# Optimization experiments

Measured on AMD Instinct MI355X. Metric: run time of the kernel, lower is better.

## Reference

```python
import jax, jax.numpy as jnp
from jax import lax
import numpy as np

B, C, H, W = 8, 32, 512, 256
HEAD = 64
NUM_PEAKS, RADIUS, THRESH = 18, 5, 0.1
BN_EPS = 1e-5


def setup_inputs() -> dict:
    key = jax.random.key(0)
    ks = jax.random.split(key, 8)
    f32 = jnp.float32
    return {
        "x": jax.random.normal(ks[0], (B, C, H, W), f32),
        # fc_hm head params
        "w1_hm": jax.random.normal(ks[1], (HEAD, C, 3, 3), f32) * 0.05,
        "b1_hm": jnp.zeros((HEAD,), f32),
        "g_hm": jnp.ones((HEAD,), f32),
        "be_hm": jnp.zeros((HEAD,), f32),
        "m_hm": jnp.zeros((HEAD,), f32),
        "v_hm": jnp.ones((HEAD,), f32),
        "w2_hm": jax.random.normal(ks[2], (2, HEAD, 1, 1), f32) * 0.05,
        "b2_hm": jnp.zeros((2,), f32),
        # fc_vec head params
        "w1_vec": jax.random.normal(ks[3], (HEAD, C, 3, 3), f32) * 0.05,
        "b1_vec": jnp.zeros((HEAD,), f32),
        "g_vec": jnp.ones((HEAD,), f32),
        "be_vec": jnp.zeros((HEAD,), f32),
        "m_vec": jnp.zeros((HEAD,), f32),
        "v_vec": jnp.ones((HEAD,), f32),
        "w2_vec": jax.random.normal(ks[4], (2, HEAD, 1, 1), f32) * 0.05,
        "b2_vec": jnp.zeros((2,), f32),
    }


def _conv(x, w, b):
    y = lax.conv_general_dilated(x, w, (1, 1), 'SAME',
                                 dimension_numbers=('NCHW', 'OIHW', 'NCHW'))
    return y + b[None, :, None, None]


def _head(x, w1, b1, g, be, m, v, w2, b2):
    # conv3x3 -> BN(eval) -> ReLU -> (dropout=identity) -> conv final_kernel
    h = _conv(x, w1, b1)
    h = g[None, :, None, None] * (h - m[None, :, None, None]) \
        * lax.rsqrt(v + BN_EPS)[None, :, None, None] + be[None, :, None, None]
    h = jax.nn.relu(h)
    return _conv(h, w2, b2)


def _extract_peaks(hm):
    # hm: [H, W] -> peaks [NUM_PEAKS, 2] as (x, y); iterative argmax + square suppression
    ys = jnp.arange(H)[:, None]
    xs = jnp.arange(W)[None, :]

    def step(hmw, _):
        flat = hmw.reshape(-1)
        idx = jnp.argmax(flat)
        mval = flat[idx]
        y = idx // W
        x = idx % W
        valid = mval > THRESH
        peak = jnp.where(valid,
                         jnp.stack([x, y]).astype(hmw.dtype),
                         jnp.zeros((2,), hmw.dtype))
        sup = (jnp.abs(ys - y) <= RADIUS) & (jnp.abs(xs - x) <= RADIUS)
        hmw = jnp.where(valid & sup, jnp.zeros((), hmw.dtype), hmw)
        return hmw, peak

    _, peaks = lax.scan(step, hm, None, length=NUM_PEAKS)
    return peaks


def _order_points(points):
    # points: [N, 2]; pack valid points sorted by y descending, zeros at the end
    valid = points.sum(axis=1) != 0
    key_y = jnp.where(valid, points[:, 1], -jnp.inf)
    order = jnp.argsort(-key_y)
    p = points[order]
    return jnp.where(valid[order][:, None], p, jnp.zeros((), p.dtype))


def reference(x, w1_hm, b1_hm, g_hm, be_hm, m_hm, v_hm, w2_hm, b2_hm,
              w1_vec, b1_vec, g_vec, be_vec, m_vec, v_vec, w2_vec, b2_vec):
    dual_hm = jax.nn.sigmoid(_head(x, w1_hm, b1_hm, g_hm, be_hm, m_hm, v_hm, w2_hm, b2_hm))  # [B,2,H,W]
    vec_ind = _head(x, w1_vec, b1_vec, g_vec, be_vec, m_vec, v_vec, w2_vec, b2_vec)          # [B,2,H,W]

    peaks = jax.vmap(_extract_peaks)(dual_hm.reshape(B * 2, H, W)).reshape(B, 2, NUM_PEAKS, 2)
    upper = jax.vmap(_order_points)(peaks[:, 0])  # [B,18,2]
    lower = jax.vmap(_order_points)(peaks[:, 1])  # [B,18,2]
    mid = (upper + lower) / 2
    return dual_hm, upper, lower, mid, vec_ind
```

## Files before the change

kernel.cpp:

```cpp
#include <hip/hip_runtime.h>

typedef _Float16 f16;
typedef _Float16 f16x8 __attribute__((ext_vector_type(8)));
typedef float f32x4 __attribute__((ext_vector_type(4)));

#define Bn 8
#define Him 512
#define Wim 256
#define NPK 18
#define RAD 5
#define PTHRESH 0.1f
#define BN_EPS 1e-5f

#define SZ_HM   (Bn*2*Him*Wim)
#define OFF_UP  (SZ_HM)
#define OFF_LO  (OFF_UP + Bn*NPK*2)
#define OFF_MID (OFF_LO + Bn*NPK*2)
#define OFF_VEC (OFF_MID + Bn*NPK*2)

#define PH (Him + 2)
#define PW (Wim + 2)
#define XH_ELT ((size_t)Bn * PH * PW * 32)
#define XH_BYTES (XH_ELT * 2)
#define WBYTES 73728
#define WS_NEED (XH_BYTES + WBYTES + 4096)

#define WS_WBYTES 73728
#define XCOLS 258
#define XSTR  40


__global__ __launch_bounds__(256) void xform_kernel(
    const float* __restrict__ x, f16* __restrict__ xh)
{
    int e = blockIdx.x * 256 + threadIdx.x;
    if (e >= Bn * PH * PW * 4) return;
    int cb  = e & 3;
    int pxl = e >> 2;
    int b   = pxl / (PH * PW);
    int rem = pxl - b * (PH * PW);
    int yy  = rem / PW;
    int xx  = rem - yy * PW;
    int yv = yy - 1, xv = xx - 1;
    f16x8 hv;
    if ((unsigned)yv < (unsigned)Him && (unsigned)xv < (unsigned)Wim) {
        const float* sp = x + (((size_t)b * 32 + cb * 8) * Him + yv) * Wim + xv;
#pragma unroll
        for (int j = 0; j < 8; ++j) hv[j] = (f16)sp[(size_t)j * Him * Wim];
    } else {
#pragma unroll
        for (int j = 0; j < 8; ++j) hv[j] = (f16)0.f;
    }
    *(f16x8*)&xh[(size_t)pxl * 32 + cb * 8] = hv;
}

__global__ __launch_bounds__(256) void prep4_kernel(
    const float* __restrict__ w1_hm, const float* __restrict__ b1_hm,
    const float* __restrict__ g_hm,  const float* __restrict__ be_hm,
    const float* __restrict__ m_hm,  const float* __restrict__ v_hm,
    const float* __restrict__ w1_vec, const float* __restrict__ b1_vec,
    const float* __restrict__ g_vec,  const float* __restrict__ be_vec,
    const float* __restrict__ m_vec,  const float* __restrict__ v_vec,
    const float* __restrict__ w2_hm,  const float* __restrict__ w2_vec,
    void* __restrict__ wreg)
{
    f16* wf = (f16*)wreg;
    float* btf = (float*)((char*)wreg + WBYTES);
    float* waf = btf + 128;
    float* wbf = btf + 256;

    int e = blockIdx.x * 256 + threadIdx.x;
    int rs = e >> 12;
    int rem = e & 4095;
    int n = rem >> 5;
    int c = rem & 31;

    float g, vv, v;
    if (n < 64) { g = g_hm[n]; vv = v_hm[n]; v = w1_hm[(n * 32 + c) * 9 + rs]; }
    else { int j = n - 64; g = g_vec[j]; vv = v_vec[j]; v = w1_vec[(j * 32 + c) * 9 + rs]; }
    float al = g * rsqrtf(vv + BN_EPS);
    int byte = rs * 8192 + n * 64 + c * 2;
    byte ^= (n & 7) << 4;
    wf[byte >> 1] = (f16)(v * al);

    if (e < 128) {
        int nn = e;
        float gg, be, m, vvv, b1;
        if (nn < 64) { gg = g_hm[nn]; be = be_hm[nn]; m = m_hm[nn]; vvv = v_hm[nn]; b1 = b1_hm[nn]; }
        else { int j = nn - 64; gg = g_vec[j]; be = be_vec[j]; m = m_vec[j]; vvv = v_vec[j]; b1 = b1_vec[j]; }
        float a = gg * rsqrtf(vvv + BN_EPS);
        btf[nn] = a * (b1 - m) + be;
        if (nn < 64) { waf[nn] = w2_hm[nn]; wbf[nn] = w2_hm[64 + nn]; }
        else { int j = nn - 64; waf[nn] = w2_vec[j]; wbf[nn] = w2_vec[64 + j]; }
    }
}

__global__ __launch_bounds__(512, 2) void conv7_kernel(
    const f16* __restrict__ xh, const f16* __restrict__ wsw,
    const float* __restrict__ btf, const float* __restrict__ waf,
    const float* __restrict__ wbf,
    const float* __restrict__ b2_hm, const float* __restrict__ b2_vec,
    float* __restrict__ out)
{
    __shared__ __align__(16) f16 s_w[9 * 128 * 32];
    __shared__ __align__(16) f16 s_in[10 * 130 * 32];

    const int hw = blockIdx.x;
    const int logical = (hw & 7) * 128 + (hw >> 3);
    const int b    = logical >> 7;
    const int idx  = logical & 127;
    const int strip = idx >> 1;
    const int half  = idx & 1;
    const int y0  = strip * 8;
    const int x0h = half * 128;

    const int tid  = threadIdx.x;
    const int lane = tid & 63;
    const int wv   = tid >> 6;

    {
        const float4* src = (const float4*)wsw;
        float4* dst = (float4*)s_w;
#pragma unroll
        for (int i = 0; i < 9; ++i) dst[tid + 512 * i] = src[tid + 512 * i];
    }
    {
        const char* xb = (const char*)(xh + (size_t)b * PH * (PW * 32));
        char* sb = (char*)s_in;
        for (int i = tid; i < 5200; i += 512) {
            int row = i / 520;
            int r2  = i - row * 520;
            int px  = r2 >> 2;
            int bo  = (r2 & 3) << 4;
            f16x8 v = *(const f16x8*)(xb + (((size_t)(y0 + row) * PW + (x0h + px)) << 6) + bo);
            int la = ((row * 130 + px) << 6) + bo;
            la ^= (px & 7) << 4;
            *(f16x8*)(sb + la) = v;
        }
    }
    __syncthreads();

    const int l15 = lane & 15;
    const int g   = lane >> 4;
    const int khB = g << 4;
    const int sxz = ((l15 << 6) + khB) ^ ((l15 & 7) << 4);
    const char* swb = (const char*)s_w;
    const char* sib = (const char*)s_in;

    float* outhm  = out + ((size_t)b * 2) * Him * Wim + (y0 + wv) * Wim + x0h;
    float* outvec = out + OFF_VEC + ((size_t)b * 2) * Him * Wim + (y0 + wv) * Wim + x0h;

#pragma unroll 1
    for (int xseg = 0; xseg < 2; ++xseg) {
        const int px0s = xseg << 6;

        f32x4 acc[8][4];
#pragma unroll
        for (int ct = 0; ct < 8; ++ct)
#pragma unroll
            for (int nt = 0; nt < 4; ++nt) acc[ct][nt] = (f32x4){0.f, 0.f, 0.f, 0.f};

#pragma unroll 1
        for (int rr = 0; rr < 3; ++rr) {
#pragma unroll 1
            for (int ss = 0; ss < 3; ++ss) {
                f16x8 af[4];
#pragma unroll
                for (int nt = 0; nt < 4; ++nt) {
                    int pxl = px0s + nt * 16 + l15 + ss;
                    int la = (((wv + rr) * 130 + pxl) << 6) + khB;
                    la ^= (pxl & 7) << 4;
                    af[nt] = *(const f16x8*)(sib + la);
                }
                const char* wtap = swb + (rr * 3 + ss) * 8192 + sxz;
#pragma unroll
                for (int ct = 0; ct < 8; ++ct) {
                    f16x8 wfr = *(const f16x8*)(wtap + ct * 1024);
                    acc[ct][0] = __builtin_amdgcn_mfma_f32_16x16x32_f16(wfr, af[0], acc[ct][0], 0, 0, 0);
                    acc[ct][1] = __builtin_amdgcn_mfma_f32_16x16x32_f16(wfr, af[1], acc[ct][1], 0, 0, 0);
                    acc[ct][2] = __builtin_amdgcn_mfma_f32_16x16x32_f16(wfr, af[2], acc[ct][2], 0, 0, 0);
                    acc[ct][3] = __builtin_amdgcn_mfma_f32_16x16x32_f16(wfr, af[3], acc[ct][3], 0, 0, 0);
                }
            }
        }

        float s[4][4];
#pragma unroll
        for (int nt = 0; nt < 4; ++nt)
#pragma unroll
            for (int o = 0; o < 4; ++o) s[nt][o] = 0.f;

        const int cb0 = g << 2;
#pragma unroll
        for (int ct = 0; ct < 8; ++ct) {
            const float4 bt4 = *(const float4*)&btf[ct * 16 + cb0];
            const float4 wa4 = *(const float4*)&waf[ct * 16 + cb0];
            const float4 wb4 = *(const float4*)&wbf[ct * 16 + cb0];
            float btq[4] = { bt4.x, bt4.y, bt4.z, bt4.w };
            float waq[4] = { wa4.x, wa4.y, wa4.z, wa4.w };
            float wbq[4] = { wb4.x, wb4.y, wb4.z, wb4.w };
#pragma unroll
            for (int nt = 0; nt < 4; ++nt) {
#pragma unroll
                for (int q = 0; q < 4; ++q) {
                    float h = fmaxf(acc[ct][nt][q] + btq[q], 0.f);
                    if (ct < 4) {
                        s[nt][0] = fmaf(waq[q], h, s[nt][0]);
                        s[nt][1] = fmaf(wbq[q], h, s[nt][1]);
                    } else {
                        s[nt][2] = fmaf(waq[q], h, s[nt][2]);
                        s[nt][3] = fmaf(wbq[q], h, s[nt][3]);
                    }
                }
            }
        }
#pragma unroll
        for (int nt = 0; nt < 4; ++nt)
#pragma unroll
            for (int o = 0; o < 4; ++o) {
                s[nt][o] += __shfl_xor(s[nt][o], 16);
                s[nt][o] += __shfl_xor(s[nt][o], 32);
            }

        const float bh0 = b2_hm[0], bh1 = b2_hm[1], bv0 = b2_vec[0], bv1 = b2_vec[1];
        if (g == 0) {
#pragma unroll
            for (int nt = 0; nt < 4; ++nt) {
                int px = px0s + nt * 16 + l15;
                float e = __expf(-(s[nt][0] + bh0));
                outhm[px] = 1.f / (1.f + e);
            }
        } else if (g == 1) {
#pragma unroll
            for (int nt = 0; nt < 4; ++nt) {
                int px = px0s + nt * 16 + l15;
                float e = __expf(-(s[nt][1] + bh1));
                outhm[Him * Wim + px] = 1.f / (1.f + e);
            }
        } else if (g == 2) {
#pragma unroll
            for (int nt = 0; nt < 4; ++nt) {
                int px = px0s + nt * 16 + l15;
                outvec[px] = s[nt][2] + bv0;
            }
        } else {
#pragma unroll
            for (int nt = 0; nt < 4; ++nt) {
                int px = px0s + nt * 16 + l15;
                outvec[Him * Wim + px] = s[nt][3] + bv1;
            }
        }
    }
}


__global__ __launch_bounds__(256) void prep_fb_kernel(
    const float* __restrict__ w1_hm, const float* __restrict__ b1_hm,
    const float* __restrict__ g_hm,  const float* __restrict__ be_hm,
    const float* __restrict__ m_hm,  const float* __restrict__ v_hm,
    const float* __restrict__ w1_vec, const float* __restrict__ b1_vec,
    const float* __restrict__ g_vec,  const float* __restrict__ be_vec,
    const float* __restrict__ m_vec,  const float* __restrict__ v_vec,
    void* __restrict__ wsv)
{
    f16* wf = (f16*)wsv;
    float* alpha = (float*)((char*)wsv + WS_WBYTES);
    float* beta  = alpha + 128;
    int e = blockIdx.x * 256 + threadIdx.x;
    int rs = e >> 12;
    int rem = e & 4095;
    int n = rem >> 5;
    int c = rem & 31;
    float v;
    if (n < 64) v = w1_hm[(n * 32 + c) * 9 + rs];
    else        v = w1_vec[((n - 64) * 32 + c) * 9 + rs];
    wf[e] = (f16)v;
    if (e < 128) {
        int nn = e;
        float g, be, m, vv, b1;
        if (nn < 64) { g = g_hm[nn]; be = be_hm[nn]; m = m_hm[nn]; vv = v_hm[nn]; b1 = b1_hm[nn]; }
        else { int j = nn - 64; g = g_vec[j]; be = be_vec[j]; m = m_vec[j]; vv = v_vec[j]; b1 = b1_vec[j]; }
        float a = g * rsqrtf(vv + BN_EPS);
        alpha[nn] = a;
        beta[nn]  = a * (b1 - m) + be;
    }
}

__global__ __launch_bounds__(256, 1) void conv_fb_kernel(
    const float* __restrict__ x, const void* __restrict__ wsv,
    const float* __restrict__ w2_hm, const float* __restrict__ b2_hm,
    const float* __restrict__ w2_vec, const float* __restrict__ b2_vec,
    float* __restrict__ out)
{
    __shared__ __align__(16) f16 s_x[3 * XCOLS * XSTR];
    __shared__ __align__(16) f16 s_w[9 * 128 * 32];

    const int bid = blockIdx.x;
    const int y = bid & 511;
    const int b = bid >> 9;
    const int tid = threadIdx.x;
    const int lane = tid & 63;
    const int wv = tid >> 6;

    {
        const float4* src = (const float4*)wsv;
        float4* dst = (float4*)s_w;
#pragma unroll
        for (int i = 0; i < 18; ++i) dst[tid + 256 * i] = src[tid + 256 * i];
    }
    {
        const float* xb = x + (size_t)b * 32 * Him * Wim;
#pragma unroll 1
        for (int g = 0; g < 12; ++g) {
            int r  = g >> 2;
            int cb = (g & 3) << 3;
            int gy = y + r - 1;
            bool rowok = (gy >= 0) && (gy < Him);
            {
                int col = tid;
                int gx = col - 1;
                bool ok = rowok && (gx >= 0);
                f16x8 hv;
#pragma unroll
                for (int j = 0; j < 8; ++j) {
                    float v = ok ? xb[(size_t)(cb + j) * (Him * Wim) + gy * Wim + gx] : 0.f;
                    hv[j] = (f16)v;
                }
                *(f16x8*)&s_x[(r * XCOLS + col) * XSTR + cb] = hv;
            }
            if (tid < 2) {
                int col = 256 + tid;
                int gx = col - 1;
                bool ok = rowok && (gx < Wim);
                f16x8 hv;
#pragma unroll
                for (int j = 0; j < 8; ++j) {
                    float v = ok ? xb[(size_t)(cb + j) * (Him * Wim) + gy * Wim + gx] : 0.f;
                    hv[j] = (f16)v;
                }
                *(f16x8*)&s_x[(r * XCOLS + col) * XSTR + cb] = hv;
            }
        }
    }
    __syncthreads();

    const int px0 = wv * 64;
    const int l15 = lane & 15;
    const int khalf = (lane >> 4) << 3;

    f32x4 acc[4][8];
#pragma unroll
    for (int pt = 0; pt < 4; ++pt)
#pragma unroll
        for (int nt = 0; nt < 8; ++nt) acc[pt][nt] = (f32x4){0.f, 0.f, 0.f, 0.f};

#pragma unroll 1
    for (int rs = 0; rs < 9; ++rs) {
        const int rr = rs / 3, ss = rs % 3;
        f16x8 af[4];
#pragma unroll
        for (int pt = 0; pt < 4; ++pt) {
            int col = px0 + pt * 16 + l15 + ss;
            af[pt] = *(const f16x8*)&s_x[(rr * XCOLS + col) * XSTR + khalf];
        }
#pragma unroll
        for (int nt = 0; nt < 8; ++nt) {
            f16x8 bf = *(const f16x8*)&s_w[rs * 4096 + (nt * 16 + l15) * 32 + khalf];
            acc[0][nt] = __builtin_amdgcn_mfma_f32_16x16x32_f16(af[0], bf, acc[0][nt], 0, 0, 0);
            acc[1][nt] = __builtin_amdgcn_mfma_f32_16x16x32_f16(af[1], bf, acc[1][nt], 0, 0, 0);
            acc[2][nt] = __builtin_amdgcn_mfma_f32_16x16x32_f16(af[2], bf, acc[2][nt], 0, 0, 0);
            acc[3][nt] = __builtin_amdgcn_mfma_f32_16x16x32_f16(af[3], bf, acc[3][nt], 0, 0, 0);
        }
    }

    const float* alpha = (const float*)((const char*)wsv + WS_WBYTES);
    const float* beta  = alpha + 128;
    float al[8], bt[8], wa[8], wb[8];
#pragma unroll
    for (int nt = 0; nt < 8; ++nt) {
        int ch = nt * 16 + l15;
        al[nt] = alpha[ch];
        bt[nt] = beta[ch];
        int c6 = ch & 63;
        const float* w2 = (ch < 64) ? w2_hm : w2_vec;
        wa[nt] = w2[c6];
        wb[nt] = w2[64 + c6];
    }
    const float bh0 = b2_hm[0], bh1 = b2_hm[1], bv0 = b2_vec[0], bv1 = b2_vec[1];

    float* outhm  = out + ((size_t)b * 2) * Him * Wim + y * Wim;
    float* outvec = out + OFF_VEC + ((size_t)b * 2) * Him * Wim + y * Wim;

#pragma unroll
    for (int pt = 0; pt < 4; ++pt) {
#pragma unroll
        for (int q = 0; q < 4; ++q) {
            float s0 = 0.f, s1 = 0.f, s2 = 0.f, s3 = 0.f;
#pragma unroll
            for (int nt = 0; nt < 8; ++nt) {
                float h = fmaf(al[nt], acc[pt][nt][q], bt[nt]);
                h = fmaxf(h, 0.f);
                if (nt < 4) { s0 = fmaf(wa[nt], h, s0); s1 = fmaf(wb[nt], h, s1); }
                else        { s2 = fmaf(wa[nt], h, s2); s3 = fmaf(wb[nt], h, s3); }
            }
#pragma unroll
            for (int off = 1; off < 16; off <<= 1) {
                s0 += __shfl_xor(s0, off);
                s1 += __shfl_xor(s1, off);
                s2 += __shfl_xor(s2, off);
                s3 += __shfl_xor(s3, off);
            }
            int px = px0 + pt * 16 + ((lane >> 4) << 2) + q;
            if (l15 == 0) {
                outhm[px] = 1.f / (1.f + expf(-(s0 + bh0)));
            } else if (l15 == 1) {
                outhm[Him * Wim + px] = 1.f / (1.f + expf(-(s1 + bh1)));
            } else if (l15 == 2) {
                outvec[px] = s2 + bv0;
            } else if (l15 == 3) {
                outvec[Him * Wim + px] = s3 + bv1;
            }
        }
    }
}

__global__ __launch_bounds__(1024) void peak_kernel(float* __restrict__ out)
{
    __shared__ float rowval[512];
    __shared__ int   rowcol[512];
    __shared__ int   sbx[NPK], sby[NPK];
    __shared__ int   ppx[NPK], ppy[NPK];

    int m = blockIdx.x;
    const float* hm = out + (size_t)m * (Him * Wim);
    int tid  = threadIdx.x;
    int lane = tid & 63;
    int wv   = tid >> 6;

    if (tid < NPK) { ppx[tid] = 0; ppy[tid] = 0; }

#pragma unroll 4
    for (int row = wv; row < 512; row += 16) {
        float4 v4 = *reinterpret_cast<const float4*>(hm + row * 256 + (lane << 2));
        float bv = v4.x; int bc = lane << 2;
        if (v4.y > bv) { bv = v4.y; bc = (lane << 2) + 1; }
        if (v4.z > bv) { bv = v4.z; bc = (lane << 2) + 2; }
        if (v4.w > bv) { bv = v4.w; bc = (lane << 2) + 3; }
#pragma unroll
        for (int off = 32; off; off >>= 1) {
            float ov = __shfl_xor(bv, off);
            int   oc = __shfl_xor(bc, off);
            if (ov > bv || (ov == bv && oc < bc)) { bv = ov; bc = oc; }
        }
        if (lane == 0) { rowval[row] = bv; rowcol[row] = bc; }
    }
    __syncthreads();

    if (wv != 0) return;

    for (int it = 0; it < NPK; ++it) {
        float bv = rowval[lane]; int br = lane;
#pragma unroll
        for (int k = 1; k < 8; ++k) {
            int r = lane + (k << 6);
            float v = rowval[r];
            if (v > bv) { bv = v; br = r; }
        }
#pragma unroll
        for (int off = 32; off; off >>= 1) {
            float ov = __shfl_xor(bv, off);
            int   orr = __shfl_xor(br, off);
            if (ov > bv || (ov == bv && orr < br)) { bv = ov; br = orr; }
        }
        if (!(bv > PTHRESH)) break;

        int gy = br;
        int gc = rowcol[gy];
        if (lane == 0) { ppx[it] = gc; ppy[it] = gy; sbx[it] = gc; sby[it] = gy; }
        int nb = it + 1;

        bool needy = false;
        if (lane < 11) {
            int r0 = gy - RAD + lane;
            if (r0 >= 0 && r0 < 512) {
                int d = rowcol[r0] - gc; if (d < 0) d = -d;
                needy = (d <= RAD);
            }
        }
        unsigned long long mask = __ballot(needy);

        while (mask) {
            int bit = __builtin_ctzll(mask);
            mask &= mask - 1;
            int r = gy - RAD + bit;
            float4 v4 = *reinterpret_cast<const float4*>(hm + r * 256 + (lane << 2));
            float vals[4] = { v4.x, v4.y, v4.z, v4.w };
            float bv2 = -1.f; int bc2 = 0;
#pragma unroll
            for (int q = 0; q < 4; ++q) {
                int col = (lane << 2) + q;
                float val = vals[q];
                for (int i = 0; i < nb; ++i) {
                    int dy = r - sby[i]; if (dy < 0) dy = -dy;
                    int dx = col - sbx[i]; if (dx < 0) dx = -dx;
                    if (dy <= RAD && dx <= RAD) { val = 0.f; break; }
                }
                if (val > bv2) { bv2 = val; bc2 = col; }
            }
#pragma unroll
            for (int off = 32; off; off >>= 1) {
                float ov = __shfl_xor(bv2, off);
                int   oc = __shfl_xor(bc2, off);
                if (ov > bv2 || (ov == bv2 && oc < bc2)) { bv2 = ov; bc2 = oc; }
            }
            if (lane == 0) { rowval[r] = bv2; rowcol[r] = bc2; }
        }
    }

    if (tid == 0) {
        float key[NPK]; int ord[NPK];
        for (int i = 0; i < NPK; ++i) {
            int valid = (ppx[i] + ppy[i]) != 0;
            key[i] = valid ? (float)ppy[i] : -3.4e38f;
            ord[i] = i;
        }
        for (int i = 1; i < NPK; ++i) {
            int oi = ord[i]; float ki = key[oi];
            int j = i - 1;
            while (j >= 0 && key[ord[j]] < ki) { ord[j + 1] = ord[j]; --j; }
            ord[j + 1] = oi;
        }
        int bb = m >> 1, which = m & 1;
        float* dst = out + (which ? OFF_LO : OFF_UP) + bb * (NPK * 2);
        for (int i = 0; i < NPK; ++i) {
            int src = ord[i];
            int valid = (ppx[src] + ppy[src]) != 0;
            dst[i * 2 + 0] = valid ? (float)ppx[src] : 0.f;
            dst[i * 2 + 1] = valid ? (float)ppy[src] : 0.f;
        }
    }
}

__global__ __launch_bounds__(320) void mid_kernel(float* __restrict__ out)
{
    int t = threadIdx.x;
    if (t < Bn * NPK * 2)
        out[OFF_MID + t] = 0.5f * (out[OFF_UP + t] + out[OFF_LO + t]);
}

extern "C" void kernel_launch(void* const* d_in, const int* in_sizes, int n_in,
                              void* d_out, int out_size, void* d_ws, size_t ws_size,
                              hipStream_t stream)
{
    const float* x      = (const float*)d_in[0];
    const float* w1_hm  = (const float*)d_in[1];
    const float* b1_hm  = (const float*)d_in[2];
    const float* g_hm   = (const float*)d_in[3];
    const float* be_hm  = (const float*)d_in[4];
    const float* m_hm   = (const float*)d_in[5];
    const float* v_hm   = (const float*)d_in[6];
    const float* w2_hm  = (const float*)d_in[7];
    const float* b2_hm  = (const float*)d_in[8];
    const float* w1_vec = (const float*)d_in[9];
    const float* b1_vec = (const float*)d_in[10];
    const float* g_vec  = (const float*)d_in[11];
    const float* be_vec = (const float*)d_in[12];
    const float* m_vec  = (const float*)d_in[13];
    const float* v_vec  = (const float*)d_in[14];
    const float* w2_vec = (const float*)d_in[15];
    const float* b2_vec = (const float*)d_in[16];

    float* out = (float*)d_out;

    if (ws_size >= (size_t)WS_NEED) {
        f16*  xh   = (f16*)d_ws;
        char* wreg = (char*)d_ws + XH_BYTES;
        const float* btf = (const float*)(wreg + WBYTES);
        const float* waf = btf + 128;
        const float* wbf = btf + 256;

        xform_kernel<<<(Bn * PH * PW * 4 + 255) / 256, 256, 0, stream>>>(x, xh);
        prep4_kernel<<<144, 256, 0, stream>>>(
            w1_hm, b1_hm, g_hm, be_hm, m_hm, v_hm,
            w1_vec, b1_vec, g_vec, be_vec, m_vec, v_vec,
            w2_hm, w2_vec, wreg);
        conv7_kernel<<<1024, 512, 0, stream>>>(
            xh, (const f16*)wreg, btf, waf, wbf,
            b2_hm, b2_vec, out);
    } else {
        prep_fb_kernel<<<144, 256, 0, stream>>>(
            w1_hm, b1_hm, g_hm, be_hm, m_hm, v_hm,
            w1_vec, b1_vec, g_vec, be_vec, m_vec, v_vec, d_ws);
        conv_fb_kernel<<<Bn * Him, 256, 0, stream>>>(
            x, d_ws, w2_hm, b2_hm, w2_vec, b2_vec, out);
    }

    peak_kernel<<<Bn * 2, 1024, 0, stream>>>(out);

    mid_kernel<<<1, 320, 0, stream>>>(out);
}
```

Baseline: 270.1 us.

## Split peak extraction into scan and iterate kernels with DPP reductions

Splits the peak kernel into two. A 1024-thread scan kernel writes per-row max and column to workspace, and a 64-thread iterate kernel runs the 18 sequential argmax/suppression steps. The iterate kernel prefetches all 11 candidate rows unconditionally before deciding which ones need rescanning, so load latency overlaps. Wave-wide argmax reductions now use DPP for the intra-row steps instead of shuffles throughout. This costs an extra launch and a global round trip for the row maxima, and the scan buffers reuse the start of the workspace that held the f16 input, which is safe only because the conv kernel has already finished.

```diff
diff --git a/kernel.cpp b/kernel.cpp
--- a/kernel.cpp
+++ b/kernel.cpp
@@ -28,6 +28,27 @@
 #define WS_WBYTES 73728
 #define XCOLS 258
 #define XSTR  40
+
+template <int CTRL>
+__device__ __forceinline__ void red2_dpp(float& v, int& r) {
+    int ov  = __builtin_amdgcn_update_dpp(0, __float_as_int(v), CTRL, 0xF, 0xF, true);
+    int orr = __builtin_amdgcn_update_dpp(0, r, CTRL, 0xF, 0xF, true);
+    float fv = __int_as_float(ov);
+    if (fv > v || (fv == v && orr < r)) { v = fv; r = orr; }
+}
+__device__ __forceinline__ void red2_shfl(float& v, int& r, const int off) {
+    float fv = __shfl_xor(v, off);
+    int  orr = __shfl_xor(r, off);
+    if (fv > v || (fv == v && orr < r)) { v = fv; r = orr; }
+}
+__device__ __forceinline__ void argred64(float& v, int& r) {
+    red2_dpp<0xB1>(v, r);
+    red2_dpp<0x4E>(v, r);
+    red2_dpp<0x141>(v, r);
+    red2_dpp<0x140>(v, r);
+    red2_shfl(v, r, 16);
+    red2_shfl(v, r, 32);
+}
 
 
 __global__ __launch_bounds__(256) void xform_kernel(
@@ -249,6 +270,130 @@
                 int px = px0s + nt * 16 + l15;
                 outvec[Him * Wim + px] = s[nt][3] + bv1;
             }
+        }
+    }
+}
+
+__global__ __launch_bounds__(1024) void peak_scan_kernel(
+    const float* __restrict__ out, float* __restrict__ scanv, int* __restrict__ scanc)
+{
+    int m = blockIdx.x;
+    const float* hm = out + (size_t)m * (Him * Wim);
+    int tid  = threadIdx.x;
+    int lane = tid & 63;
+    int wv   = tid >> 6;
+#pragma unroll 4
+    for (int row = wv; row < 512; row += 16) {
+        float4 v4 = *reinterpret_cast<const float4*>(hm + row * 256 + (lane << 2));
+        float bv = v4.x; int bc = lane << 2;
+        if (v4.y > bv) { bv = v4.y; bc = (lane << 2) + 1; }
+        if (v4.z > bv) { bv = v4.z; bc = (lane << 2) + 2; }
+        if (v4.w > bv) { bv = v4.w; bc = (lane << 2) + 3; }
+        argred64(bv, bc);
+        if (lane == 0) { scanv[(m << 9) + row] = bv; scanc[(m << 9) + row] = bc; }
+    }
+}
+
+__global__ __launch_bounds__(64) void peak_iter_kernel(
+    const float* __restrict__ scanv, const int* __restrict__ scanc,
+    float* __restrict__ out)
+{
+    __shared__ float s_rv[512];
+    __shared__ int   s_rc[512];
+    __shared__ int   sbx[NPK], sby[NPK];
+    __shared__ int   ppx[NPK], ppy[NPK];
+
+    int m = blockIdx.x;
+    int lane = threadIdx.x;
+    const float* hm = out + (size_t)m * (Him * Wim);
+
+#pragma unroll
+    for (int k = 0; k < 8; ++k) {
+        int r = lane + (k << 6);
+        s_rv[r] = scanv[(m << 9) + r];
+        s_rc[r] = scanc[(m << 9) + r];
+    }
+    if (lane < NPK) { ppx[lane] = 0; ppy[lane] = 0; }
+
+    for (int it = 0; it < NPK; ++it) {
+        float bv = s_rv[lane]; int br = lane;
+#pragma unroll
+        for (int k = 1; k < 8; ++k) {
+            int r = lane + (k << 6);
+            float v = s_rv[r];
+            if (v > bv) { bv = v; br = r; }
+        }
+        argred64(bv, br);
+        if (!(bv > PTHRESH)) break;
+
+        int gy = br;
+        int gc = s_rc[gy];
+        if (lane == 0) { ppx[it] = gc; ppy[it] = gy; sbx[it] = gc; sby[it] = gy; }
+        int nb = it + 1;
+
+        float4 pre[11];
+#pragma unroll
+        for (int t = 0; t < 11; ++t) {
+            int r = gy - RAD + t;
+            if (r >= 0 && r < 512)
+                pre[t] = *reinterpret_cast<const float4*>(hm + r * 256 + (lane << 2));
+            else
+                pre[t] = make_float4(0.f, 0.f, 0.f, 0.f);
+        }
+
+        bool needy = false;
+        if (lane < 11) {
+            int r0 = gy - RAD + lane;
+            if (r0 >= 0 && r0 < 512) {
+                int d = s_rc[r0] - gc; if (d < 0) d = -d;
+                needy = (d <= RAD);
+            }
+        }
+        unsigned long long mask = __ballot(needy);
+
+#pragma unroll
+        for (int t = 0; t < 11; ++t) {
+            if (mask & (1ull << t)) {
+                int r = gy - RAD + t;
+                float vals[4] = { pre[t].x, pre[t].y, pre[t].z, pre[t].w };
+                float bv2 = -1.f; int bc2 = 0;
+#pragma unroll
+                for (int q = 0; q < 4; ++q) {
+                    int col = (lane << 2) + q;
+                    float val = vals[q];
+                    for (int i = 0; i < nb; ++i) {
+                        int dy = r - sby[i]; if (dy < 0) dy = -dy;
+                        int dx = col - sbx[i]; if (dx < 0) dx = -dx;
+                        if (dy <= RAD && dx <= RAD) { val = 0.f; break; }
+                    }
+                    if (val > bv2) { bv2 = val; bc2 = col; }
+                }
+                argred64(bv2, bc2);
+                if (lane == 0) { s_rv[r] = bv2; s_rc[r] = bc2; }
+            }
+        }
+    }
+
+    if (lane == 0) {
+        float key[NPK]; int ord[NPK];
+        for (int i = 0; i < NPK; ++i) {
+            int valid = (ppx[i] + ppy[i]) != 0;
+            key[i] = valid ? (float)ppy[i] : -3.4e38f;
+            ord[i] = i;
+        }
+        for (int i = 1; i < NPK; ++i) {
+            int oi = ord[i]; float ki = key[oi];
+            int j = i - 1;
+            while (j >= 0 && key[ord[j]] < ki) { ord[j + 1] = ord[j]; --j; }
+            ord[j + 1] = oi;
+        }
+        int bb = m >> 1, which = m & 1;
+        float* dst = out + (which ? OFF_LO : OFF_UP) + bb * (NPK * 2);
+        for (int i = 0; i < NPK; ++i) {
+            int src = ord[i];
+            int valid = (ppx[src] + ppy[src]) != 0;
+            dst[i * 2 + 0] = valid ? (float)ppx[src] : 0.f;
+            dst[i * 2 + 1] = valid ? (float)ppy[src] : 0.f;
         }
     }
 }
@@ -424,7 +569,7 @@
     }
 }
 
-__global__ __launch_bounds__(1024) void peak_kernel(float* __restrict__ out)
+__global__ __launch_bounds__(1024) void peak_fb_kernel(float* __restrict__ out)
 {
     __shared__ float rowval[512];
     __shared__ int   rowcol[512];
@@ -446,12 +591,7 @@
         if (v4.y > bv) { bv = v4.y; bc = (lane << 2) + 1; }
         if (v4.z > bv) { bv = v4.z; bc = (lane << 2) + 2; }
         if (v4.w > bv) { bv = v4.w; bc = (lane << 2) + 3; }
-#pragma unroll
-        for (int off = 32; off; off >>= 1) {
-            float ov = __shfl_xor(bv, off);
-            int   oc = __shfl_xor(bc, off);
-            if (ov > bv || (ov == bv && oc < bc)) { bv = ov; bc = oc; }
-        }
+        argred64(bv, bc);
         if (lane == 0) { rowval[row] = bv; rowcol[row] = bc; }
     }
     __syncthreads();
@@ -466,12 +606,7 @@
             float v = rowval[r];
             if (v > bv) { bv = v; br = r; }
         }
-#pragma unroll
-        for (int off = 32; off; off >>= 1) {
-            float ov = __shfl_xor(bv, off);
-            int   orr = __shfl_xor(br, off);
-            if (ov > bv || (ov == bv && orr < br)) { bv = ov; br = orr; }
-        }
+        argred64(bv, br);
         if (!(bv > PTHRESH)) break;
 
         int gy = br;
@@ -507,12 +642,7 @@
                 }
                 if (val > bv2) { bv2 = val; bc2 = col; }
             }
-#pragma unroll
-            for (int off = 32; off; off >>= 1) {
-                float ov = __shfl_xor(bv2, off);
-                int   oc = __shfl_xor(bc2, off);
-                if (ov > bv2 || (ov == bv2 && oc < bc2)) { bv2 = ov; bc2 = oc; }
-            }
+            argred64(bv2, bc2);
             if (lane == 0) { rowval[r] = bv2; rowcol[r] = bc2; }
         }
     }
@@ -587,15 +717,19 @@
         conv7_kernel<<<1024, 512, 0, stream>>>(
             xh, (const f16*)wreg, btf, waf, wbf,
             b2_hm, b2_vec, out);
+
+        float* scanv = (float*)d_ws;
+        int*   scanc = (int*)((char*)d_ws + 32768);
+        peak_scan_kernel<<<Bn * 2, 1024, 0, stream>>>(out, scanv, scanc);
+        peak_iter_kernel<<<Bn * 2, 64, 0, stream>>>(scanv, scanc, out);
     } else {
         prep_fb_kernel<<<144, 256, 0, stream>>>(
             w1_hm, b1_hm, g_hm, be_hm, m_hm, v_hm,
             w1_vec, b1_vec, g_vec, be_vec, m_vec, v_vec, d_ws);
         conv_fb_kernel<<<Bn * Him, 256, 0, stream>>>(
             x, d_ws, w2_hm, b2_hm, w2_vec, b2_vec, out);
-    }
-
-    peak_kernel<<<Bn * 2, 1024, 0, stream>>>(out);
+        peak_fb_kernel<<<Bn * 2, 1024, 0, stream>>>(out);
+    }
 
     mid_kernel<<<1, 320, 0, stream>>>(out);
 }
```

New measurement: 282.3 us. 4.5% more time.
